# Performance work log

Hardware: AMD Instinct MI355X
Metric: run time of the kernel (lower is better)

Reference implementation:

```python
import jax, jax.numpy as jnp
import numpy as np

B, T, C, H = 2, 2048, 1024, 16
HS = C // H  # head_size = 64
EPS = 1e-5


def _layernorm(x, w, b):
    mu = jnp.mean(x, axis=-1, keepdims=True)
    var = jnp.mean(jnp.square(x - mu), axis=-1, keepdims=True)
    return (x - mu) * jax.lax.rsqrt(var + EPS) * w + b


def setup_inputs() -> dict:
    key = jax.random.key(0)
    ks = jax.random.split(key, 12)
    s_attn = 1.0 / np.sqrt(C)
    s_ff1 = 1.0 / np.sqrt(C)
    s_ff2 = 1.0 / np.sqrt(4 * C)
    return {
        "x": jax.random.normal(ks[0], (B, T, C), dtype=jnp.float32),
        "ln1_w": jnp.ones((C,), jnp.float32),
        "ln1_b": jnp.zeros((C,), jnp.float32),
        "Wq": jax.random.normal(ks[1], (H, C, HS), jnp.float32) * s_attn,
        "Wk": jax.random.normal(ks[2], (H, C, HS), jnp.float32) * s_attn,
        "Wv": jax.random.normal(ks[3], (H, C, HS), jnp.float32) * s_attn,
        "proj_w": jax.random.normal(ks[4], (C, C), jnp.float32) * s_attn,
        "proj_b": jnp.zeros((C,), jnp.float32),
        "ln2_w": jnp.ones((C,), jnp.float32),
        "ln2_b": jnp.zeros((C,), jnp.float32),
        "fc1_w": jax.random.normal(ks[5], (C, 4 * C), jnp.float32) * s_ff1,
        "fc1_b": jnp.zeros((4 * C,), jnp.float32),
        "fc2_w": jax.random.normal(ks[6], (4 * C, C), jnp.float32) * s_ff2,
        "fc2_b": jnp.zeros((C,), jnp.float32),
    }


def reference(x, ln1_w, ln1_b, Wq, Wk, Wv, proj_w, proj_b, ln2_w, ln2_b, fc1_w, fc1_b, fc2_w, fc2_b):
    Bx, Tx, Cx = x.shape
    # --- self-attention with pre-norm residual ---
    h = _layernorm(x, ln1_w, ln1_b)                       # [B,T,C]
    q = jnp.einsum("btc,hcd->bhtd", h, Wq)                 # [B,H,T,HS]
    k = jnp.einsum("btc,hcd->bhtd", h, Wk)
    v = jnp.einsum("btc,hcd->bhtd", h, Wv)
    # NOTE: original code applies NO 1/sqrt(d) scaling -- keep faithful.
    wei = jnp.einsum("bhtd,bhsd->bhts", q, k)              # [B,H,T,T]
    causal = jnp.tril(jnp.ones((Tx, Tx), dtype=bool))
    wei = jnp.where(causal, wei, -jnp.inf)
    wei = jax.nn.softmax(wei, axis=-1)
    attn = jnp.einsum("bhts,bhsd->bhtd", wei, v)           # [B,H,T,HS]
    attn = attn.transpose(0, 2, 1, 3).reshape(Bx, Tx, Cx)  # concat heads
    sa = attn @ proj_w + proj_b                            # output projection
    x = x + sa
    # --- FFN with pre-norm residual ---
    h2 = _layernorm(x, ln2_w, ln2_b)
    ff = jax.nn.relu(h2 @ fc1_w + fc1_b) @ fc2_w + fc2_b
    return x + ff
```

## Files before the change

kernel.cpp:

```cpp
#include <hip/hip_runtime.h>
#include <hip/hip_bf16.h>

#define Bn 2
#define Tn 2048
#define Cn 1024
#define Hn 16
#define HSn 64
#define Mn (Bn*Tn)
#define LN_EPS 1e-5f

typedef unsigned short u16;
typedef __attribute__((ext_vector_type(8))) short bf16x8;
typedef __attribute__((ext_vector_type(4))) float f32x4;

#define MFMA16(a,b,c) __builtin_amdgcn_mfma_f32_16x16x32_bf16(a, b, c, 0, 0, 0)
#define GLL16(g,l) __builtin_amdgcn_global_load_lds( \
    (const __attribute__((address_space(1))) void*)(g), \
    (__attribute__((address_space(3))) void*)(l), 16, 0, 0)

__device__ __forceinline__ u16 f2b(float f) {
    unsigned int u = __float_as_uint(f);
    unsigned int r = (u + 0x7FFFu + ((u >> 16) & 1u)) >> 16;
    return (u16)r;
}
__device__ __forceinline__ float b2f(unsigned u) {
    return __uint_as_float(u << 16);
}
__device__ __forceinline__ unsigned cvtpk(float lo, float hi) {
    unsigned r;
    asm("v_cvt_pk_bf16_f32 %0, %1, %2" : "=v"(r) : "v"(lo), "v"(hi));
    return r;
}

__global__ __launch_bounds__(256) void wqkv_t(
    const float* __restrict__ Wq, const float* __restrict__ Wk,
    const float* __restrict__ Wv, u16* __restrict__ Wt)
{
    int z = blockIdx.z, h = blockIdx.y, c0 = blockIdx.x * 64;
    const float* in = (z == 0 ? Wq : z == 1 ? Wk : Wv) + (size_t)h * 65536;
    __shared__ float t[64][68];
    int tid = threadIdx.x;
#pragma unroll
    for (int it = 0; it < 4; it++) {
        int r = it * 16 + (tid >> 4);
        *(float4*)&t[r][(tid & 15) * 4] =
            *(const float4*)(in + (size_t)(c0 + r) * 64 + (tid & 15) * 4);
    }
    __syncthreads();
    int d = tid >> 2, seg = tid & 3;
    union { u16 u[8]; uint4 q; } pk;
#pragma unroll
    for (int hq = 0; hq < 2; hq++) {
#pragma unroll
        for (int j = 0; j < 8; j++) pk.u[j] = f2b(t[seg * 16 + hq * 8 + j][d]);
        *(uint4*)(Wt + (size_t)(z * 1024 + h * 64 + d) * 1024 + c0 + seg * 16 + hq * 8) = pk.q;
    }
}

__global__ __launch_bounds__(256) void transpose_cvt(
    const float* __restrict__ in, u16* __restrict__ out, int R, int C)
{
    __shared__ float t[64][68];
    int r0 = blockIdx.y * 64, c0 = blockIdx.x * 64;
    int tid = threadIdx.x;
#pragma unroll
    for (int it = 0; it < 4; it++) {
        int r = it * 16 + (tid >> 4);
        *(float4*)&t[r][(tid & 15) * 4] =
            *(const float4*)(in + (size_t)(r0 + r) * C + c0 + (tid & 15) * 4);
    }
    __syncthreads();
    int c = tid >> 2, seg = tid & 3;
    union { u16 u[8]; uint4 q; } pk;
#pragma unroll
    for (int hq = 0; hq < 2; hq++) {
#pragma unroll
        for (int j = 0; j < 8; j++) pk.u[j] = f2b(t[seg * 16 + hq * 8 + j][c]);
        *(uint4*)(out + (size_t)(c0 + c) * R + r0 + seg * 16 + hq * 8) = pk.q;
    }
}

__global__ __launch_bounds__(256) void ln_bf16(
    const float* __restrict__ x, const float* __restrict__ w,
    const float* __restrict__ bvec, u16* __restrict__ out)
{
    int row  = blockIdx.x * 4 + (threadIdx.x >> 6);
    int lane = threadIdx.x & 63;
    const float* xr = x + (size_t)row * Cn;
    float4 v[4];
    float s = 0.f, sq = 0.f;
#pragma unroll
    for (int i = 0; i < 4; i++) {
        v[i] = *(const float4*)(xr + lane * 4 + i * 256);
        s  += v[i].x + v[i].y + v[i].z + v[i].w;
        sq += v[i].x * v[i].x + v[i].y * v[i].y + v[i].z * v[i].z + v[i].w * v[i].w;
    }
#pragma unroll
    for (int off = 1; off < 64; off <<= 1) {
        s  += __shfl_xor(s, off);
        sq += __shfl_xor(sq, off);
    }
    float mu   = s * (1.f / Cn);
    float var  = sq * (1.f / Cn) - mu * mu;
    float rstd = rsqrtf(var + LN_EPS);
    u16* orow = out + (size_t)row * Cn;
#pragma unroll
    for (int i = 0; i < 4; i++) {
        float4 w4 = *(const float4*)(w    + lane * 4 + i * 256);
        float4 b4 = *(const float4*)(bvec + lane * 4 + i * 256);
        union { u16 u[4]; uint2 q; } pk;
        pk.u[0] = f2b((v[i].x - mu) * rstd * w4.x + b4.x);
        pk.u[1] = f2b((v[i].y - mu) * rstd * w4.y + b4.y);
        pk.u[2] = f2b((v[i].z - mu) * rstd * w4.z + b4.z);
        pk.u[3] = f2b((v[i].w - mu) * rstd * w4.w + b4.w);
        *(uint2*)(orow + lane * 4 + i * 256) = pk.q;
    }
}

template<int OBF, int BIAS, int RELU>
__global__ __launch_bounds__(512, 2) void gemm_8ph(
    const u16* __restrict__ A, const u16* __restrict__ Bt,
    const float* __restrict__ bias, void* Cout,
    int M, int N, int K, int NT)
{
    __shared__ u16 lds[65536];
    const int tid = threadIdx.x, l = tid & 63, w = tid >> 6;
    const int wm = w >> 2, wn = w & 3;
    const int g = l >> 4, c16 = l & 15;

    const int nwg = (int)gridDim.x, cpx = nwg >> 3;
    const int bid = (int)blockIdx.x;
    const int sbid = (bid & 7) * cpx + (bid >> 3);
    const int m0 = (sbid / NT) * 256, n0 = (sbid % NT) * 256;

    const int sr = tid >> 3;
    const int ss = ((tid & 7) ^ (sr & 7)) << 3;
    const u16* Asrc = A  + (size_t)(m0 + sr) * K + ss;
    const u16* Bsrc = Bt + (size_t)(n0 + sr) * K + ss;
    const int dst0 = tid * 8;

#define ST_A8(d_, h_, kt_) do {                                              \
        GLL16(Asrc + (size_t)((h_) * 128) * K + (size_t)(kt_) * 64,          \
              &lds[(d_) * 32768 + (h_) * 8192 + dst0]);                      \
        GLL16(Asrc + (size_t)((h_) * 128 + 64) * K + (size_t)(kt_) * 64,     \
              &lds[(d_) * 32768 + (h_) * 8192 + 4096 + dst0]);               \
    } while (0)
#define ST_B8(d_, h_, kt_) do {                                              \
        GLL16(Bsrc + (size_t)((h_) * 128) * K + (size_t)(kt_) * 64,          \
              &lds[(d_) * 32768 + 16384 + (h_) * 8192 + dst0]);              \
        GLL16(Bsrc + (size_t)((h_) * 128 + 64) * K + (size_t)(kt_) * 64,     \
              &lds[(d_) * 32768 + 16384 + (h_) * 8192 + 4096 + dst0]);       \
    } while (0)
#define LDA8(d_, mi_, s_) (*(const bf16x8*)&lds[(d_) * 32768 +               \
        (wm * 128 + (mi_) * 16 + c16) * 64 +                                  \
        ((((s_) * 4 + g) ^ ((wm * 128 + (mi_) * 16 + c16) & 7)) << 3)])
#define LDB8(d_, nj_, s_) (*(const bf16x8*)&lds[(d_) * 32768 + 16384 +       \
        (wn * 64 + (nj_) * 16 + c16) * 64 +                                   \
        ((((s_) * 4 + g) ^ ((wn * 64 + (nj_) * 16 + c16) & 7)) << 3)])
#define PH_HEAD() do {                                                       \
        __builtin_amdgcn_s_barrier();                                        \
        asm volatile("s_waitcnt lgkmcnt(0)" ::: "memory");                   \
        __builtin_amdgcn_sched_barrier(0);                                   \
        __builtin_amdgcn_s_setprio(1);                                       \
    } while (0)
#define PH_MFMA(NH_) do {                                                    \
        _Pragma("unroll")                                                    \
        for (int mi = 0; mi < 8; mi++) {                                     \
            acc[mi][2*(NH_)]   = MFMA16(aF[mi], bF[0], acc[mi][2*(NH_)]);    \
            acc[mi][2*(NH_)+1] = MFMA16(aF[mi], bF[1], acc[mi][2*(NH_)+1]);  \
        }                                                                    \
    } while (0)

    f32x4 acc[8][4];
#pragma unroll
    for (int i = 0; i < 8; i++)
#pragma unroll
        for (int j = 0; j < 4; j++) acc[i][j] = (f32x4){0.f, 0.f, 0.f, 0.f};

    const int nk = K >> 6;
    ST_A8(0, 0, 0); ST_A8(0, 1, 0); ST_B8(0, 0, 0); ST_B8(0, 1, 0);
    ST_A8(1, 0, 1); ST_A8(1, 1, 1);
    asm volatile("s_waitcnt vmcnt(4)" ::: "memory");
    __builtin_amdgcn_s_barrier();

    bf16x8 aF[8], bF[2];
    for (int m = 0; m < nk; m++) {
        const int d = m & 1, dn = d ^ 1;
#pragma unroll
        for (int mi = 0; mi < 8; mi++) aF[mi] = LDA8(d, mi, 0);
        bF[0] = LDB8(d, 0, 0); bF[1] = LDB8(d, 1, 0);
        if (m + 1 < nk) ST_B8(dn, 0, m + 1);
        PH_HEAD(); PH_MFMA(0);
        __builtin_amdgcn_s_setprio(0);
        __builtin_amdgcn_s_barrier();
        bF[0] = LDB8(d, 2, 0); bF[1] = LDB8(d, 3, 0);
        if (m + 1 < nk) ST_B8(dn, 1, m + 1);
        PH_HEAD(); PH_MFMA(1);
        __builtin_amdgcn_s_setprio(0);
        __builtin_amdgcn_s_barrier();
#pragma unroll
        for (int mi = 0; mi < 8; mi++) aF[mi] = LDA8(d, mi, 1);
        bF[0] = LDB8(d, 0, 1); bF[1] = LDB8(d, 1, 1);
        PH_HEAD(); PH_MFMA(0);
        __builtin_amdgcn_s_setprio(0);
        __builtin_amdgcn_s_barrier();
        bF[0] = LDB8(d, 2, 1); bF[1] = LDB8(d, 3, 1);
        if (m + 2 < nk) { ST_A8(d, 0, m + 2); ST_A8(d, 1, m + 2); }
        PH_HEAD(); PH_MFMA(1);
        __builtin_amdgcn_s_setprio(0);
        if (m + 1 < nk) {
            if (m + 2 < nk) asm volatile("s_waitcnt vmcnt(4)" ::: "memory");
            else            asm volatile("s_waitcnt vmcnt(0)" ::: "memory");
        }
        __builtin_amdgcn_s_barrier();
    }
#undef ST_A8
#undef ST_B8
#undef LDA8
#undef LDB8
#undef PH_HEAD
#undef PH_MFMA

#pragma unroll
    for (int mi = 0; mi < 8; mi++)
#pragma unroll
        for (int nj = 0; nj < 4; nj++) {
            const int coln = n0 + wn * 64 + nj * 16 + c16;
            float bv = BIAS ? bias[coln] : 0.f;
#pragma unroll
            for (int reg = 0; reg < 4; reg++) {
                int rowm = m0 + wm * 128 + mi * 16 + 4 * g + reg;
                float v = acc[mi][nj][reg] + bv;
                if (RELU) v = fmaxf(v, 0.f);
                if (OBF) ((u16*)Cout)[(size_t)rowm * N + coln] = f2b(v);
                else     ((float*)Cout)[(size_t)rowm * N + coln] = v;
            }
        }
}

__global__ __launch_bounds__(512, 2) void gemm_fc2(
    const u16* __restrict__ A, const u16* __restrict__ Bt,
    u16* __restrict__ part)
{
    __shared__ u16 lds[65536];
    const int tid = threadIdx.x, l = tid & 63, w = tid >> 6;
    const int wm = w >> 2, wn = w & 3;
    const int g = l >> 4, c16 = l & 15;

    const int bid = (int)blockIdx.x;
    const int sbid = (bid & 7) * 32 + (bid >> 3);
    const int chunk = sbid >> 6, t = sbid & 63;
    const int m0 = (t >> 2) * 256, n0 = (t & 3) * 256;
    const int kB = chunk << 10;

    const int sr = tid >> 3;
    const int ss = ((tid & 7) ^ (sr & 7)) << 3;
    const u16* Asrc = A  + (size_t)(m0 + sr) * 4096 + kB + ss;
    const u16* Bsrc = Bt + (size_t)(n0 + sr) * 4096 + kB + ss;
    const int dst0 = tid * 8;

#define ST_A8(d_, h_, kt_) do {                                              \
        GLL16(Asrc + (size_t)((h_) * 128) * 4096 + (size_t)(kt_) * 64,       \
              &lds[(d_) * 32768 + (h_) * 8192 + dst0]);                      \
        GLL16(Asrc + (size_t)((h_) * 128 + 64) * 4096 + (size_t)(kt_) * 64,  \
              &lds[(d_) * 32768 + (h_) * 8192 + 4096 + dst0]);               \
    } while (0)
#define ST_B8(d_, h_, kt_) do {                                              \
        GLL16(Bsrc + (size_t)((h_) * 128) * 4096 + (size_t)(kt_) * 64,       \
              &lds[(d_) * 32768 + 16384 + (h_) * 8192 + dst0]);              \
        GLL16(Bsrc + (size_t)((h_) * 128 + 64) * 4096 + (size_t)(kt_) * 64,  \
              &lds[(d_) * 32768 + 16384 + (h_) * 8192 + 4096 + dst0]);       \
    } while (0)
#define LDA8(d_, mi_, s_) (*(const bf16x8*)&lds[(d_) * 32768 +               \
        (wm * 128 + (mi_) * 16 + c16) * 64 +                                  \
        ((((s_) * 4 + g) ^ ((wm * 128 + (mi_) * 16 + c16) & 7)) << 3)])
#define LDB8(d_, nj_, s_) (*(const bf16x8*)&lds[(d_) * 32768 + 16384 +       \
        (wn * 64 + (nj_) * 16 + c16) * 64 +                                   \
        ((((s_) * 4 + g) ^ ((wn * 64 + (nj_) * 16 + c16) & 7)) << 3)])
#define PH_HEAD() do {                                                       \
        __builtin_amdgcn_s_barrier();                                        \
        asm volatile("s_waitcnt lgkmcnt(0)" ::: "memory");                   \
        __builtin_amdgcn_sched_barrier(0);                                   \
        __builtin_amdgcn_s_setprio(1);                                       \
    } while (0)
#define PH_MFMA(NH_) do {                                                    \
        _Pragma("unroll")                                                    \
        for (int mi = 0; mi < 8; mi++) {                                     \
            acc[mi][2*(NH_)]   = MFMA16(aF[mi], bF[0], acc[mi][2*(NH_)]);    \
            acc[mi][2*(NH_)+1] = MFMA16(aF[mi], bF[1], acc[mi][2*(NH_)+1]);  \
        }                                                                    \
    } while (0)

    f32x4 acc[8][4];
#pragma unroll
    for (int i = 0; i < 8; i++)
#pragma unroll
        for (int j = 0; j < 4; j++) acc[i][j] = (f32x4){0.f, 0.f, 0.f, 0.f};

    const int nk = 16;
    ST_A8(0, 0, 0); ST_A8(0, 1, 0); ST_B8(0, 0, 0); ST_B8(0, 1, 0);
    ST_A8(1, 0, 1); ST_A8(1, 1, 1);
    asm volatile("s_waitcnt vmcnt(4)" ::: "memory");
    __builtin_amdgcn_s_barrier();

    bf16x8 aF[8], bF[2];
    for (int m = 0; m < nk; m++) {
        const int d = m & 1, dn = d ^ 1;
#pragma unroll
        for (int mi = 0; mi < 8; mi++) aF[mi] = LDA8(d, mi, 0);
        bF[0] = LDB8(d, 0, 0); bF[1] = LDB8(d, 1, 0);
        if (m + 1 < nk) ST_B8(dn, 0, m + 1);
        PH_HEAD(); PH_MFMA(0);
        __builtin_amdgcn_s_setprio(0);
        __builtin_amdgcn_s_barrier();
        bF[0] = LDB8(d, 2, 0); bF[1] = LDB8(d, 3, 0);
        if (m + 1 < nk) ST_B8(dn, 1, m + 1);
        PH_HEAD(); PH_MFMA(1);
        __builtin_amdgcn_s_setprio(0);
        __builtin_amdgcn_s_barrier();
#pragma unroll
        for (int mi = 0; mi < 8; mi++) aF[mi] = LDA8(d, mi, 1);
        bF[0] = LDB8(d, 0, 1); bF[1] = LDB8(d, 1, 1);
        PH_HEAD(); PH_MFMA(0);
        __builtin_amdgcn_s_setprio(0);
        __builtin_amdgcn_s_barrier();
        bF[0] = LDB8(d, 2, 1); bF[1] = LDB8(d, 3, 1);
        if (m + 2 < nk) { ST_A8(d, 0, m + 2); ST_A8(d, 1, m + 2); }
        PH_HEAD(); PH_MFMA(1);
        __builtin_amdgcn_s_setprio(0);
        if (m + 1 < nk) {
            if (m + 2 < nk) asm volatile("s_waitcnt vmcnt(4)" ::: "memory");
            else            asm volatile("s_waitcnt vmcnt(0)" ::: "memory");
        }
        __builtin_amdgcn_s_barrier();
    }
#undef ST_A8
#undef ST_B8
#undef LDA8
#undef LDB8
#undef PH_HEAD
#undef PH_MFMA

    u16* pp = part + (size_t)chunk * 4194304;
#pragma unroll
    for (int mi = 0; mi < 8; mi++)
#pragma unroll
        for (int nj = 0; nj < 4; nj++) {
            const int coln = n0 + wn * 64 + nj * 16 + c16;
#pragma unroll
            for (int reg = 0; reg < 4; reg++) {
                int rowm = m0 + wm * 128 + mi * 16 + 4 * g + reg;
                pp[(size_t)rowm * 1024 + coln] = f2b(acc[mi][nj][reg]);
            }
        }
}

__global__ __launch_bounds__(256) void splitk_reduce(
    const u16* __restrict__ part, const float* __restrict__ bias,
    float* __restrict__ out)
{
    size_t i = ((size_t)blockIdx.x * 256 + threadIdx.x) * 4;
    int col = (int)(i & 1023);
    float4 o  = *(float4*)(out + i);
    float4 bv = *(const float4*)(bias + col);
    float s0 = o.x + bv.x, s1 = o.y + bv.y, s2 = o.z + bv.z, s3 = o.w + bv.w;
#pragma unroll
    for (int c = 0; c < 4; c++) {
        uint2 p = *(const uint2*)(part + (size_t)c * 4194304 + i);
        s0 += b2f(p.x & 0xffffu);
        s1 += b2f(p.x >> 16);
        s2 += b2f(p.y & 0xffffu);
        s3 += b2f(p.y >> 16);
    }
    float4 r; r.x = s0; r.y = s1; r.z = s2; r.w = s3;
    *(float4*)(out + i) = r;
}

template<int OBF, int BIAS, int RES, int RELU>
__global__ __launch_bounds__(256) void gemm_n64(
    const u16* __restrict__ A, const u16* __restrict__ Bt,
    const float* __restrict__ bias, const float* res,
    void* Cout, int M, int N, int K)
{
    __shared__ u16 As[2][8192];
    __shared__ u16 Bs[2][4096];
    const int tid = threadIdx.x;
    const int l = tid & 63, w = tid >> 6;
    const int wr = w >> 1, wc = w & 1;
    const int g = l >> 4, c16 = l & 15;
    const int m0 = blockIdx.y * 128, n0 = blockIdx.x * 64;

    const u16* a_src[4];
    int a_dst[4];
#pragma unroll
    for (int i = 0; i < 4; i++) {
        int G = tid + 256 * i, r = G >> 3, sl = G & 7;
        a_src[i] = A + (size_t)(m0 + r) * K + ((sl ^ (r & 7)) << 3);
        a_dst[i] = G * 8;
    }
    const u16* b_src[2];
    int b_dst[2];
#pragma unroll
    for (int i = 0; i < 2; i++) {
        int G = tid + 256 * i, r = G >> 3, sl = G & 7;
        b_src[i] = Bt + (size_t)(n0 + r) * K + ((sl ^ (r & 7)) << 3);
        b_dst[i] = G * 8;
    }

    f32x4 acc[4][2];
#pragma unroll
    for (int i = 0; i < 4; i++)
#pragma unroll
        for (int j = 0; j < 2; j++) acc[i][j] = (f32x4){0.f, 0.f, 0.f, 0.f};

#define STAGE_N64(nb, k0) do {                                   \
        GLL16(a_src[0] + (k0), &As[nb][a_dst[0]]);               \
        GLL16(a_src[1] + (k0), &As[nb][a_dst[1]]);               \
        GLL16(a_src[2] + (k0), &As[nb][a_dst[2]]);               \
        GLL16(a_src[3] + (k0), &As[nb][a_dst[3]]);               \
        GLL16(b_src[0] + (k0), &Bs[nb][b_dst[0]]);               \
        GLL16(b_src[1] + (k0), &Bs[nb][b_dst[1]]);               \
    } while (0)

    STAGE_N64(0, 0);
    __syncthreads();

    int cur = 0;
    for (int k0 = 0; k0 < K; k0 += 64) {
        if (k0 + 64 < K) STAGE_N64(cur ^ 1, k0 + 64);
        const u16* AsC = As[cur];
        const u16* BsC = Bs[cur];
        bf16x8 af[4][2], bfr[2][2];
#pragma unroll
        for (int fi = 0; fi < 4; fi++) {
            int r = wr * 64 + fi * 16 + c16;
            af[fi][0] = *(const bf16x8*)&AsC[r * 64 + (((g    ) ^ (r & 7)) << 3)];
            af[fi][1] = *(const bf16x8*)&AsC[r * 64 + (((4 + g) ^ (r & 7)) << 3)];
        }
#pragma unroll
        for (int fj = 0; fj < 2; fj++) {
            int r = wc * 32 + fj * 16 + c16;
            bfr[fj][0] = *(const bf16x8*)&BsC[r * 64 + (((g    ) ^ (r & 7)) << 3)];
            bfr[fj][1] = *(const bf16x8*)&BsC[r * 64 + (((4 + g) ^ (r & 7)) << 3)];
        }
#pragma unroll
        for (int fi = 0; fi < 4; fi++)
#pragma unroll
            for (int fj = 0; fj < 2; fj++) {
                acc[fi][fj] = MFMA16(af[fi][0], bfr[fj][0], acc[fi][fj]);
                acc[fi][fj] = MFMA16(af[fi][1], bfr[fj][1], acc[fi][fj]);
            }
        __syncthreads();
        cur ^= 1;
    }
#undef STAGE_N64

#pragma unroll
    for (int fi = 0; fi < 4; fi++)
#pragma unroll
        for (int fj = 0; fj < 2; fj++) {
            int coln = n0 + wc * 32 + fj * 16 + c16;
            float bv = BIAS ? bias[coln] : 0.f;
#pragma unroll
            for (int reg = 0; reg < 4; reg++) {
                int rowm = m0 + wr * 64 + fi * 16 + 4 * g + reg;
                float v = acc[fi][fj][reg] + bv;
                if (RES) v += res[(size_t)rowm * N + coln];
                if (RELU) v = fmaxf(v, 0.f);
                if (OBF) ((u16*)Cout)[(size_t)rowm * N + coln] = f2b(v);
                else     ((float*)Cout)[(size_t)rowm * N + coln] = v;
            }
        }
}

__global__ __launch_bounds__(256) void v_transpose(
    const u16* __restrict__ qkv, u16* __restrict__ vT)
{
    int t0 = blockIdx.x * 64, h = blockIdx.y, b = blockIdx.z;
    __shared__ u16 t[64][72];
    int tid = threadIdx.x;
#pragma unroll
    for (int it = 0; it < 2; it++) {
        int r = it * 32 + (tid >> 3);
        int cs = (tid & 7) * 8;
        *(uint4*)&t[r][cs] =
            *(const uint4*)(qkv + (size_t)(b * 2048 + t0 + r) * 3072 + 2048 + h * 64 + cs);
    }
    __syncthreads();
    int d = tid >> 2, seg = tid & 3;
    union { u16 u[8]; uint4 q; } pk;
#pragma unroll
    for (int hq = 0; hq < 2; hq++) {
#pragma unroll
        for (int j = 0; j < 8; j++) pk.u[j] = t[seg * 16 + hq * 8 + j][d];
        *(uint4*)(vT + (size_t)((b * 16 + h) * 64 + d) * 2048 + t0 + seg * 16 + hq * 8) = pk.q;
    }
}

__global__ __launch_bounds__(512) void attn_mfma(
    const u16* __restrict__ qkv, const u16* __restrict__ vT,
    u16* __restrict__ outb)
{
    __shared__ u16 smem[24576];
    u16* KsB = smem;
    u16* VsB = smem + 8192;
    u16* PsB = smem + 16384;
    const int tid = threadIdx.x, l = tid & 63, w = tid >> 6;
    const int g = l >> 4, c16 = l & 15;
    const int qg = w & 3, kg = w >> 2;
    const int kg32 = kg * 32, kg64 = kg * 64;
    const int bh = blockIdx.y, b = bh >> 4, h = bh & 15;
    const int bx = (int)blockIdx.x;
    const int qt = (bh < 16) ? (15 - bx) : bx;
    const int r0 = qt * 128;
    const int wq0 = r0 + qg * 32;

    bf16x8 qf[2][2];
#pragma unroll
    for (int grp = 0; grp < 2; grp++) {
        const u16* qrow = qkv + (size_t)(b * 2048 + wq0 + grp * 16 + c16) * 3072 + h * 64;
        qf[grp][0] = *(const bf16x8*)(qrow + g * 8);
        qf[grp][1] = *(const bf16x8*)(qrow + 32 + g * 8);
    }

    const int kr = tid >> 3, ks = (tid & 7) ^ (kr & 7);
    const u16* kgp = qkv + (size_t)(b * 2048) * 3072 + 1024 + h * 64;
    const u16* vgp = vT + (size_t)((b * 16 + h) * 64) * 2048;

    float lrow[2] = {0.f, 0.f};
    f32x4 oacc[2][4];
#pragma unroll
    for (int grp = 0; grp < 2; grp++)
#pragma unroll
        for (int i = 0; i < 4; i++) oacc[grp][i] = (f32x4){0.f, 0.f, 0.f, 0.f};

    const int prow0 = (qg * 32 + c16) * 128;
    const int swz   = (c16 & 7) << 4;

#define STAGE_KV(nb, s0) do {                                                  \
        GLL16(kgp + (size_t)((s0) + kr) * 3072 + ks * 8, &KsB[(nb)*4096 + tid*8]); \
        GLL16(vgp + (size_t)kr * 2048 + (s0) + ks * 8, &VsB[(nb)*4096 + tid*8]);   \
    } while (0)

    STAGE_KV(0, 0);
    asm volatile("s_waitcnt vmcnt(0)" ::: "memory");
    __builtin_amdgcn_sched_barrier(0);
    __builtin_amdgcn_s_barrier();

    const int nt = 2 * qt + 2;
    int cur = 0;
    for (int kt = 0; kt < nt; kt++) {
        if (kt + 1 < nt) STAGE_KV(cur ^ 1, (kt + 1) * 64);
        if (kt > 0) {
            if (kt + 1 < nt) asm volatile("s_waitcnt vmcnt(2)" ::: "memory");
            else             asm volatile("s_waitcnt vmcnt(0)" ::: "memory");
            __builtin_amdgcn_sched_barrier(0);
            __builtin_amdgcn_s_barrier();
        }
        const u16* KsC = &KsB[cur * 4096];
        const u16* VsC = &VsB[cur * 4096];
        const int s0 = kt * 64;

        bf16x8 kf0[2], kf1[2];
#pragma unroll
        for (int fj = 0; fj < 2; fj++) {
            int r = kg32 + fj * 16 + c16;
            kf0[fj] = *(const bf16x8*)&KsC[r * 64 + ((g       ^ (r & 7)) << 3)];
            kf1[fj] = *(const bf16x8*)&KsC[r * 64 + (((4 + g) ^ (r & 7)) << 3)];
        }
#pragma unroll
        for (int grp = 0; grp < 2; grp++) {
            f32x4 sc[2];
            sc[0] = (f32x4){0.f, 0.f, 0.f, 0.f};
            sc[1] = (f32x4){0.f, 0.f, 0.f, 0.f};
#pragma unroll
            for (int fj = 0; fj < 2; fj++) {
                sc[fj] = MFMA16(kf0[fj], qf[grp][0], sc[fj]);
                sc[fj] = MFMA16(kf1[fj], qf[grp][1], sc[fj]);
            }
            const int qgl = wq0 + grp * 16 + c16;
            if (s0 + kg32 + 31 > wq0 + grp * 16) {
#pragma unroll
                for (int fj = 0; fj < 2; fj++)
#pragma unroll
                    for (int reg = 0; reg < 4; reg++)
                        if (s0 + kg32 + fj * 16 + 4 * g + reg > qgl)
                            sc[fj][reg] = -1e30f;
            }
#pragma unroll
            for (int fj = 0; fj < 2; fj++) {
                float p0 = __expf(sc[fj][0]);
                float p1 = __expf(sc[fj][1]);
                float p2 = __expf(sc[fj][2]);
                float p3 = __expf(sc[fj][3]);
                lrow[grp] += (p0 + p1) + (p2 + p3);
                uint2 pk;
                pk.x = cvtpk(p0, p1);
                pk.y = cvtpk(p2, p3);
                *(uint2*)((char*)PsB + prow0 + grp * 2048 +
                          ((kg64 + fj * 32 + 8 * g) ^ swz)) = pk;
            }
        }
        bf16x8 pa0 = *(const bf16x8*)((const char*)PsB + prow0 +
                                      ((kg64 + 16 * g) ^ swz));
        bf16x8 pa1 = *(const bf16x8*)((const char*)PsB + prow0 + 2048 +
                                      ((kg64 + 16 * g) ^ swz));
#pragma unroll
        for (int fd = 0; fd < 4; fd++) {
            int r = fd * 16 + c16;
            bf16x8 vf = *(const bf16x8*)&VsC[r * 64 + (((4 * kg + g) ^ (r & 7)) << 3)];
            oacc[0][fd] = MFMA16(pa0, vf, oacc[0][fd]);
            oacc[1][fd] = MFMA16(pa1, vf, oacc[1][fd]);
        }
        __builtin_amdgcn_s_barrier();
        cur ^= 1;
    }
#undef STAGE_KV

#pragma unroll
    for (int grp = 0; grp < 2; grp++) {
        lrow[grp] += __shfl_xor(lrow[grp], 16);
        lrow[grp] += __shfl_xor(lrow[grp], 32);
    }

    __syncthreads();
    float* scr = (float*)smem;
    const int sbase = qg * 2304 + l * 36;
    if (kg == 1) {
#pragma unroll
        for (int grp = 0; grp < 2; grp++) {
#pragma unroll
            for (int fd = 0; fd < 4; fd++)
                *(f32x4*)&scr[sbase + grp * 16 + fd * 4] = oacc[grp][fd];
            scr[sbase + 32 + grp] = lrow[grp];
        }
    }
    __syncthreads();
    if (kg == 0) {
#pragma unroll
        for (int grp = 0; grp < 2; grp++) {
#pragma unroll
            for (int fd = 0; fd < 4; fd++)
                oacc[grp][fd] += *(const f32x4*)&scr[sbase + grp * 16 + fd * 4];
            float lr = lrow[grp] + scr[sbase + 32 + grp];
#pragma unroll
            for (int reg = 0; reg < 4; reg++) {
                float ls = __shfl(lr, 4 * g + reg);
                float inv = 1.0f / ls;
                int t = wq0 + grp * 16 + 4 * g + reg;
                u16* op = outb + (size_t)(b * 2048 + t) * 1024 + h * 64;
#pragma unroll
                for (int fd = 0; fd < 4; fd++)
                    op[fd * 16 + c16] = f2b(oacc[grp][fd][reg] * inv);
            }
        }
    }
}

extern "C" void kernel_launch(void* const* d_in, const int* in_sizes, int n_in,
                              void* d_out, int out_size, void* d_ws, size_t ws_size,
                              hipStream_t stream) {
    const float* x     = (const float*)d_in[0];
    const float* ln1w  = (const float*)d_in[1];
    const float* ln1b  = (const float*)d_in[2];
    const float* Wq    = (const float*)d_in[3];
    const float* Wk    = (const float*)d_in[4];
    const float* Wv    = (const float*)d_in[5];
    const float* projw = (const float*)d_in[6];
    const float* projb = (const float*)d_in[7];
    const float* ln2w  = (const float*)d_in[8];
    const float* ln2b  = (const float*)d_in[9];
    const float* fc1w  = (const float*)d_in[10];
    const float* fc1b  = (const float*)d_in[11];
    const float* fc2w  = (const float*)d_in[12];
    const float* fc2b  = (const float*)d_in[13];
    float* out = (float*)d_out;

    u16* h_bf    = (u16*)d_ws;
    u16* qkv_bf  = h_bf    + 4194304;
    u16* vTb     = qkv_bf  + 12582912;
    u16* attn_bf = vTb     + 4194304;
    u16* ff1_bf  = attn_bf + 4194304;
    u16* WtQKV   = ff1_bf  + 16777216;
    u16* WtP     = WtQKV   + 3145728;
    u16* Wt1     = WtP     + 1048576;
    u16* Wt2     = Wt1     + 4194304;
    u16* fc2p = (u16*)d_ws;

    wqkv_t<<<dim3(16, 16, 3), 256, 0, stream>>>(Wq, Wk, Wv, WtQKV);
    transpose_cvt<<<dim3(16, 16), 256, 0, stream>>>(projw, WtP, 1024, 1024);
    transpose_cvt<<<dim3(64, 16), 256, 0, stream>>>(fc1w, Wt1, 1024, 4096);
    transpose_cvt<<<dim3(16, 64), 256, 0, stream>>>(fc2w, Wt2, 4096, 1024);

    ln_bf16<<<1024, 256, 0, stream>>>(x, ln1w, ln1b, h_bf);
    gemm_8ph<1, 0, 0><<<dim3(192), 512, 0, stream>>>(
        h_bf, WtQKV, nullptr, qkv_bf, Mn, 3072, 1024, 12);
    v_transpose<<<dim3(32, 16, 2), 256, 0, stream>>>(qkv_bf, vTb);
    attn_mfma<<<dim3(16, 32), 512, 0, stream>>>(qkv_bf, vTb, attn_bf);
    gemm_n64<0, 1, 1, 0><<<dim3(16, 32), 256, 0, stream>>>(
        attn_bf, WtP, projb, x, out, Mn, 1024, 1024);
    ln_bf16<<<1024, 256, 0, stream>>>(out, ln2w, ln2b, h_bf);
    gemm_8ph<1, 1, 1><<<dim3(256), 512, 0, stream>>>(
        h_bf, Wt1, fc1b, ff1_bf, Mn, 4096, 1024, 16);
    gemm_fc2<<<dim3(256), 512, 0, stream>>>(ff1_bf, Wt2, fc2p);
    splitk_reduce<<<dim3(4096), 256, 0, stream>>>(fc2p, fc2b, out);
}
```

Measured before the change: 213.5 us.

## Use dedicated 256x192-tile QKV GEMM kernel to fill all CUs

```diff
diff --git a/kernel.cpp b/kernel.cpp
--- a/kernel.cpp
+++ b/kernel.cpp
@@ -234,6 +234,120 @@
                 if (RELU) v = fmaxf(v, 0.f);
                 if (OBF) ((u16*)Cout)[(size_t)rowm * N + coln] = f2b(v);
                 else     ((float*)Cout)[(size_t)rowm * N + coln] = v;
+            }
+        }
+}
+
+__global__ __launch_bounds__(512, 1) void gemm_qkv(
+    const u16* __restrict__ A, const u16* __restrict__ Bt,
+    u16* __restrict__ Cout)
+{
+    __shared__ u16 lds[57344];
+    const int tid = threadIdx.x, l = tid & 63, w = tid >> 6;
+    const int wm = w >> 1, wn = w & 1;
+    const int g = l >> 4, c16 = l & 15;
+    const int K = 1024, N = 3072;
+
+    const int bid = (int)blockIdx.x;
+    const int sbid = (bid & 7) * 32 + (bid >> 3);
+    const int m0 = (sbid >> 4) * 256, n0 = (sbid & 15) * 192;
+
+    const int sr = tid >> 3;
+    const int ss = ((tid & 7) ^ (sr & 7)) << 3;
+    const u16* Asrc = A  + (size_t)(m0 + sr) * K + ss;
+    const u16* Bsrc = Bt + (size_t)(n0 + sr) * K + ss;
+    const int dst0 = tid * 8;
+
+#define ST_A(d_, h_, kt_) do {                                               \
+        GLL16(Asrc + (size_t)((h_) * 128) * K + (size_t)(kt_) * 64,          \
+              &lds[(d_) * 16384 + (h_) * 8192 + dst0]);                      \
+        GLL16(Asrc + (size_t)((h_) * 128 + 64) * K + (size_t)(kt_) * 64,     \
+              &lds[(d_) * 16384 + (h_) * 8192 + 4096 + dst0]);               \
+    } while (0)
+#define ST_B1(d_, seg_, kt_)                                                 \
+        GLL16(Bsrc + (size_t)((seg_) * 64) * K + (size_t)(kt_) * 64,         \
+              &lds[32768 + (d_) * 12288 + (seg_) * 4096 + dst0])
+#define LDA(d_, mi_, s_) (*(const bf16x8*)&lds[(d_) * 16384 +                \
+        (wm * 64 + (mi_) * 16 + c16) * 64 +                                   \
+        ((((s_) * 4 + g) ^ ((wm * 64 + (mi_) * 16 + c16) & 7)) << 3)])
+#define LDB(d_, nj_, s_) (*(const bf16x8*)&lds[32768 + (d_) * 12288 +        \
+        (wn * 96 + (nj_) * 16 + c16) * 64 +                                   \
+        ((((s_) * 4 + g) ^ ((wn * 96 + (nj_) * 16 + c16) & 7)) << 3)])
+#define PH_HEAD() do {                                                       \
+        __builtin_amdgcn_s_barrier();                                        \
+        asm volatile("s_waitcnt lgkmcnt(0)" ::: "memory");                   \
+        __builtin_amdgcn_sched_barrier(0);                                   \
+        __builtin_amdgcn_s_setprio(1);                                       \
+    } while (0)
+#define PH_MFMA(NH_) do {                                                    \
+        _Pragma("unroll")                                                    \
+        for (int mi = 0; mi < 4; mi++) {                                     \
+            acc[mi][3*(NH_)]   = MFMA16(aF[mi], bF[0], acc[mi][3*(NH_)]);    \
+            acc[mi][3*(NH_)+1] = MFMA16(aF[mi], bF[1], acc[mi][3*(NH_)+1]);  \
+            acc[mi][3*(NH_)+2] = MFMA16(aF[mi], bF[2], acc[mi][3*(NH_)+2]);  \
+        }                                                                    \
+    } while (0)
+
+    f32x4 acc[4][6];
+#pragma unroll
+    for (int i = 0; i < 4; i++)
+#pragma unroll
+        for (int j = 0; j < 6; j++) acc[i][j] = (f32x4){0.f, 0.f, 0.f, 0.f};
+
+    const int nk = 16;
+    ST_A(0, 0, 0); ST_A(0, 1, 0);
+    ST_B1(0, 0, 0); ST_B1(0, 1, 0); ST_B1(0, 2, 0);
+    ST_A(1, 0, 1); ST_A(1, 1, 1);
+    asm volatile("s_waitcnt vmcnt(4)" ::: "memory");
+    __builtin_amdgcn_s_barrier();
+
+    bf16x8 aF[4], bF[3];
+    for (int m = 0; m < nk; m++) {
+        const int d = m & 1, dn = d ^ 1;
+#pragma unroll
+        for (int mi = 0; mi < 4; mi++) aF[mi] = LDA(d, mi, 0);
+        bF[0] = LDB(d, 0, 0); bF[1] = LDB(d, 1, 0); bF[2] = LDB(d, 2, 0);
+        if (m + 1 < nk) { ST_B1(dn, 0, m + 1); ST_B1(dn, 1, m + 1); }
+        PH_HEAD(); PH_MFMA(0);
+        __builtin_amdgcn_s_setprio(0);
+        __builtin_amdgcn_s_barrier();
+        bF[0] = LDB(d, 3, 0); bF[1] = LDB(d, 4, 0); bF[2] = LDB(d, 5, 0);
+        if (m + 1 < nk) ST_B1(dn, 2, m + 1);
+        PH_HEAD(); PH_MFMA(1);
+        __builtin_amdgcn_s_setprio(0);
+        __builtin_amdgcn_s_barrier();
+#pragma unroll
+        for (int mi = 0; mi < 4; mi++) aF[mi] = LDA(d, mi, 1);
+        bF[0] = LDB(d, 0, 1); bF[1] = LDB(d, 1, 1); bF[2] = LDB(d, 2, 1);
+        PH_HEAD(); PH_MFMA(0);
+        __builtin_amdgcn_s_setprio(0);
+        __builtin_amdgcn_s_barrier();
+        bF[0] = LDB(d, 3, 1); bF[1] = LDB(d, 4, 1); bF[2] = LDB(d, 5, 1);
+        if (m + 2 < nk) { ST_A(d, 0, m + 2); ST_A(d, 1, m + 2); }
+        PH_HEAD(); PH_MFMA(1);
+        __builtin_amdgcn_s_setprio(0);
+        if (m + 1 < nk) {
+            if (m + 2 < nk) asm volatile("s_waitcnt vmcnt(4)" ::: "memory");
+            else            asm volatile("s_waitcnt vmcnt(0)" ::: "memory");
+        }
+        __builtin_amdgcn_s_barrier();
+    }
+#undef ST_A
+#undef ST_B1
+#undef LDA
+#undef LDB
+#undef PH_HEAD
+#undef PH_MFMA
+
+#pragma unroll
+    for (int mi = 0; mi < 4; mi++)
+#pragma unroll
+        for (int nj = 0; nj < 6; nj++) {
+            const int coln = n0 + wn * 96 + nj * 16 + c16;
+#pragma unroll
+            for (int reg = 0; reg < 4; reg++) {
+                int rowm = m0 + wm * 64 + mi * 16 + 4 * g + reg;
+                Cout[(size_t)rowm * N + coln] = f2b(acc[mi][nj][reg]);
             }
         }
 }
@@ -693,8 +807,7 @@
     transpose_cvt<<<dim3(16, 64), 256, 0, stream>>>(fc2w, Wt2, 4096, 1024);
 
     ln_bf16<<<1024, 256, 0, stream>>>(x, ln1w, ln1b, h_bf);
-    gemm_8ph<1, 0, 0><<<dim3(192), 512, 0, stream>>>(
-        h_bf, WtQKV, nullptr, qkv_bf, Mn, 3072, 1024, 12);
+    gemm_qkv<<<dim3(256), 512, 0, stream>>>(h_bf, WtQKV, qkv_bf);
     v_transpose<<<dim3(32, 16, 2), 256, 0, stream>>>(qkv_bf, vTb);
     attn_mfma<<<dim3(16, 32), 512, 0, stream>>>(qkv_bf, vTb, attn_bf);
     gemm_n64<0, 1, 1, 0><<<dim3(16, 32), 256, 0, stream>>>(
```

Result: faster. 206.1 us (-3.5%).
